# Performance work log

Hardware: AMD Instinct MI355X
Metric: run time of the kernel (lower is better)

Reference implementation:

```python
import jax, jax.numpy as jnp
import numpy as np

B, T, K = 256, 512, 128


def setup_inputs() -> dict:
    key = jax.random.key(0)
    k1, k2, k3, k4 = jax.random.split(key, 4)
    logits = jax.random.normal(k1, (B, T, K), dtype=jnp.float32)
    labels = jax.random.randint(k2, (B, T), 0, K, dtype=jnp.int32)
    seq_lens = jax.random.randint(k3, (B,), 1, T + 1, dtype=jnp.int32)
    trans = jax.random.uniform(k4, (K, K), dtype=jnp.float32)
    return {"logits": logits, "labels": labels, "seq_lens": seq_lens, "trans": trans}


def _crf_neg_log_likelihood(logits, labels, seq_lens, trans):
    # logits: [B,T,K], labels: [B,T] int, seq_lens: [B] int, trans: [K,K]
    Bb, Tt, Kk = logits.shape
    mask = (jnp.arange(Tt)[None, :] < seq_lens[:, None])  # [B,T] bool

    # ---- gold sequence score ----
    unary = jnp.take_along_axis(logits, labels[..., None].astype(jnp.int32), axis=-1)[..., 0]  # [B,T]
    unary_score = jnp.sum(jnp.where(mask, unary, 0.0), axis=-1)  # [B]
    pair = trans[labels[:, :-1], labels[:, 1:]]  # [B,T-1]
    pair_score = jnp.sum(jnp.where(mask[:, 1:], pair, 0.0), axis=-1)  # [B]
    score = unary_score + pair_score  # [B]

    # ---- log partition via forward algorithm (lax.scan over time) ----
    alpha0 = logits[:, 0]  # [B,K]
    xs = (jnp.swapaxes(logits[:, 1:], 0, 1), jnp.swapaxes(mask[:, 1:], 0, 1))  # [T-1,B,K],[T-1,B]

    def step(alpha, x):
        logit_t, m_t = x
        # alpha[:, :, None] + trans[None] : [B, K_prev, K_next]
        new = jax.nn.logsumexp(alpha[:, :, None] + trans[None, :, :], axis=1) + logit_t
        alpha = jnp.where(m_t[:, None], new, alpha)
        return alpha, None

    alpha, _ = jax.lax.scan(step, alpha0, xs)
    log_z = jax.nn.logsumexp(alpha, axis=-1)  # [B]

    log_likelihood = score - log_z
    return jnp.sum(-log_likelihood)  # scalar, matches tf.reduce_sum(-ll)


def reference(logits, labels, seq_lens, trans):
    return _crf_neg_log_likelihood(logits, labels, seq_lens, trans)
```

## Files before the change

kernel.cpp:

```cpp
#include <hip/hip_runtime.h>

#define Bdim 256
#define Tdim 512
#define Kdim 128
#define NT   128
#define CHUNK 8

typedef float v2f __attribute__((ext_vector_type(2)));

#define BAR() asm volatile("s_waitcnt lgkmcnt(0)\n\ts_barrier" ::: "memory")

template <int CTRL>
__device__ __forceinline__ float dpp_add(float v) {
    int r = __builtin_amdgcn_update_dpp(0, __float_as_int(v), CTRL, 0xF, 0xF, true);
    return v + __int_as_float(r);
}

__global__ __launch_bounds__(NT) __attribute__((amdgpu_waves_per_eu(1, 1)))
void crf_nll_kernel(
    const float* __restrict__ logits,
    const int*   __restrict__ labels,
    const int*   __restrict__ seq_lens,
    const float* __restrict__ trans,
    float* __restrict__ out)
{
    const int b   = blockIdx.x;
    const int tid = threadIdx.x;
    const int j   = tid >> 2;
    const int g   = tid & 3;
    const int L   = seq_lens[b];

    __shared__ float pbuf[2][Kdim];
    __shared__ float red2[NT / 64];

    const int*   lab_b   = labels + (size_t)b * Tdim;
    const float* logit_b = logits + (size_t)b * Tdim * Kdim;

    v2f e01[8][4], e23[8][4];
    #pragma unroll
    for (int ii = 0; ii < 8; ++ii) {
        const int f4 = (g << 3) + ((ii + j) & 7);
        #pragma unroll
        for (int ci = 0; ci < 4; ++ci) {
            const float4 tr =
                *(const float4*)&trans[(size_t)(4 * f4 + ci) * Kdim + 4 * j];
            e01[ii][ci] = (v2f){__expf(tr.x), __expf(tr.y)};
            e23[ii][ci] = (v2f){__expf(tr.z), __expf(tr.w)};
        }
    }

    float s = 0.f;
    #pragma unroll
    for (int t0 = 0; t0 < Tdim; t0 += NT) {
        const int t = t0 + tid;
        if (t < L) {
            const int lb = lab_b[t];
            s += logit_b[(size_t)t * Kdim + lb];
            if (t >= 1) s += trans[(size_t)lab_b[t - 1] * Kdim + lb];
        }
    }
    #pragma unroll
    for (int o = 32; o > 0; o >>= 1) s += __shfl_down(s, o, 64);
    if ((tid & 63) == 0) red2[tid >> 6] = s;

    pbuf[0][tid] = __expf(logit_b[tid]);
    float off = 0.f;
    int cb = 0;
    __syncthreads();
    const float score = red2[0] + red2[1];

    float curl[CHUNK], nxtl[CHUNK], ex[CHUNK];
    #pragma unroll
    for (int u = 0; u < CHUNK; ++u) {
        const int tt = 1 + u;
        curl[u] = (tt < Tdim) ? logit_b[(size_t)tt * Kdim + tid] : 0.f;
    }

#define STEP_BODY(SC_EXPR, RENORM)                                          \
    do {                                                                    \
        const float4* a4 = (const float4*)pbuf[cb];                         \
        float p0 = 1.f;                                                     \
        if (RENORM) p0 = pbuf[cb][0];                                       \
        v2f A0 = {0.f, 0.f}, A1 = {0.f, 0.f};                               \
        v2f B0 = {0.f, 0.f}, B1 = {0.f, 0.f};                               \
        _Pragma("unroll")                                                   \
        for (int ii = 0; ii < 8; ++ii) {                                    \
            const float4 p = a4[(g << 3) + ((ii + j) & 7)];                 \
            A0 = __builtin_elementwise_fma((v2f){p.x, p.x}, e01[ii][0], A0);\
            A1 = __builtin_elementwise_fma((v2f){p.x, p.x}, e23[ii][0], A1);\
            B0 = __builtin_elementwise_fma((v2f){p.y, p.y}, e01[ii][1], B0);\
            B1 = __builtin_elementwise_fma((v2f){p.y, p.y}, e23[ii][1], B1);\
            A0 = __builtin_elementwise_fma((v2f){p.z, p.z}, e01[ii][2], A0);\
            A1 = __builtin_elementwise_fma((v2f){p.z, p.z}, e23[ii][2], A1);\
            B0 = __builtin_elementwise_fma((v2f){p.w, p.w}, e01[ii][3], B0);\
            B1 = __builtin_elementwise_fma((v2f){p.w, p.w}, e23[ii][3], B1);\
        }                                                                   \
        const v2f s01 = A0 + B0;            \
        const v2f s23 = A1 + B1;            \
        float c0 = s01.x, c1 = s01.y, c2 = s23.x, c3 = s23.y;               \
        c0 = dpp_add<0xB1>(c0); c0 = dpp_add<0x4E>(c0);                     \
        c1 = dpp_add<0xB1>(c1); c1 = dpp_add<0x4E>(c1);                     \
        c2 = dpp_add<0xB1>(c2); c2 = dpp_add<0x4E>(c2);                     \
        c3 = dpp_add<0xB1>(c3); c3 = dpp_add<0x4E>(c3);                     \
        float sel  = (g & 1) ? c1 : c0;                                     \
        float selh = (g & 1) ? c3 : c2;                                     \
        sel = (g & 2) ? selh : sel;                                         \
        float anew = sel * (SC_EXPR);                                       \
        if (RENORM) {                                                       \
            const float lp0 = __logf(p0);                                   \
            anew *= __expf(-lp0);                                           \
            off  += lp0;                                                    \
        }                                                                   \
        pbuf[cb ^ 1][tid] = anew;                                           \
        cb ^= 1;                                                            \
        BAR();                                                              \
    } while (0)

    int tb = 1;
    for (; tb + CHUNK <= L; tb += CHUNK) {
        #pragma unroll
        for (int u = 0; u < CHUNK; ++u) {
            const int tt = tb + CHUNK + u;
            nxtl[u] = (tt < Tdim) ? logit_b[(size_t)tt * Kdim + tid] : 0.f;
        }
        #pragma unroll
        for (int u = 0; u < CHUNK; ++u)
            ex[u] = __expf(curl[u]);
        #pragma unroll
        for (int u = 0; u < CHUNK; ++u)
            STEP_BODY(ex[u], (u & 3) == 3);
        #pragma unroll
        for (int u = 0; u < CHUNK; ++u) curl[u] = nxtl[u];
    }
    for (int u = 0; tb + u < L; ++u)
        STEP_BODY(__expf(curl[u]), (u & 3) == 3);

#undef STEP_BODY

    __syncthreads();
    float as = pbuf[cb][tid];
    #pragma unroll
    for (int o = 32; o > 0; o >>= 1) as += __shfl_down(as, o, 64);
    __syncthreads();
    if ((tid & 63) == 0) red2[tid >> 6] = as;
    __syncthreads();
    if (tid == 0) {
        const float logz = off + __logf(red2[0] + red2[1]);
        atomicAdd(out, logz - score);
    }
}

extern "C" void kernel_launch(void* const* d_in, const int* in_sizes, int n_in,
                              void* d_out, int out_size, void* d_ws, size_t ws_size,
                              hipStream_t stream) {
    const float* logits   = (const float*)d_in[0];
    const int*   labels   = (const int*)d_in[1];
    const int*   seq_lens = (const int*)d_in[2];
    const float* trans    = (const float*)d_in[3];
    float* out = (float*)d_out;

    (void)hipMemsetAsync(out, 0, sizeof(float), stream);
    crf_nll_kernel<<<dim3(Bdim), dim3(NT), 0, stream>>>(
        logits, labels, seq_lens, trans, out);
}
```

Baseline: 268.1 us.

## Split each output column across eight lanes with 256 threads per block

Doubles the block to 256 threads so each column's 128-wide dot product is split across 8 lanes instead of 4. Each thread now holds half as many exp(trans) registers and does half the FMAs and LDS reads per step, which should shorten the serial per-timestep critical path. In exchange it adds a third DPP reduction stage, duplicate lanes that compute the same column, and a barrier spanning four waves instead of two.

```diff
diff --git a/kernel.cpp b/kernel.cpp
--- a/kernel.cpp
+++ b/kernel.cpp
@@ -3,7 +3,7 @@
 #define Bdim 256
 #define Tdim 512
 #define Kdim 128
-#define NT   128
+#define NT   256
 #define CHUNK 8
 
 typedef float v2f __attribute__((ext_vector_type(2)));
@@ -26,24 +26,25 @@
 {
     const int b   = blockIdx.x;
     const int tid = threadIdx.x;
-    const int j   = tid >> 2;
-    const int g   = tid & 3;
+    const int j4  = tid >> 3;
+    const int g   = tid & 7;
+    const int cj  = 4 * j4 + (g & 3);
     const int L   = seq_lens[b];
 
     __shared__ float pbuf[2][Kdim];
-    __shared__ float red2[NT / 64];
+    __shared__ float sred[NT / 64];
 
     const int*   lab_b   = labels + (size_t)b * Tdim;
     const float* logit_b = logits + (size_t)b * Tdim * Kdim;
 
-    v2f e01[8][4], e23[8][4];
+    v2f e01[4][4], e23[4][4];
     #pragma unroll
-    for (int ii = 0; ii < 8; ++ii) {
-        const int f4 = (g << 3) + ((ii + j) & 7);
+    for (int ii = 0; ii < 4; ++ii) {
+        const int row0 = 16 * g + (((ii + (g >> 1)) & 3) << 2);
         #pragma unroll
         for (int ci = 0; ci < 4; ++ci) {
             const float4 tr =
-                *(const float4*)&trans[(size_t)(4 * f4 + ci) * Kdim + 4 * j];
+                *(const float4*)&trans[(size_t)(row0 + ci) * Kdim + 4 * j4];
             e01[ii][ci] = (v2f){__expf(tr.x), __expf(tr.y)};
             e23[ii][ci] = (v2f){__expf(tr.z), __expf(tr.w)};
         }
@@ -61,19 +62,24 @@
     }
     #pragma unroll
     for (int o = 32; o > 0; o >>= 1) s += __shfl_down(s, o, 64);
-    if ((tid & 63) == 0) red2[tid >> 6] = s;
+    if ((tid & 63) == 0) sred[tid >> 6] = s;
 
-    pbuf[0][tid] = __expf(logit_b[tid]);
+    if (g < 4) pbuf[0][cj] = __expf(logit_b[cj]);
     float off = 0.f;
     int cb = 0;
     __syncthreads();
-    const float score = red2[0] + red2[1];
+
+    float score = 0.f;
+    if (tid == 0) {
+        #pragma unroll
+        for (int w = 0; w < NT / 64; ++w) score += sred[w];
+    }
 
     float curl[CHUNK], nxtl[CHUNK], ex[CHUNK];
     #pragma unroll
     for (int u = 0; u < CHUNK; ++u) {
         const int tt = 1 + u;
-        curl[u] = (tt < Tdim) ? logit_b[(size_t)tt * Kdim + tid] : 0.f;
+        curl[u] = (tt < Tdim) ? logit_b[(size_t)tt * Kdim + cj] : 0.f;
     }
 
 #define STEP_BODY(SC_EXPR, RENORM)                                          \
@@ -84,8 +90,8 @@
         v2f A0 = {0.f, 0.f}, A1 = {0.f, 0.f};                               \
         v2f B0 = {0.f, 0.f}, B1 = {0.f, 0.f};                               \
         _Pragma("unroll")                                                   \
-        for (int ii = 0; ii < 8; ++ii) {                                    \
-            const float4 p = a4[(g << 3) + ((ii + j) & 7)];                 \
+        for (int ii = 0; ii < 4; ++ii) {                                    \
+            const float4 p = a4[(g << 2) + ((ii + (g >> 1)) & 3)];          \
             A0 = __builtin_elementwise_fma((v2f){p.x, p.x}, e01[ii][0], A0);\
             A1 = __builtin_elementwise_fma((v2f){p.x, p.x}, e23[ii][0], A1);\
             B0 = __builtin_elementwise_fma((v2f){p.y, p.y}, e01[ii][1], B0);\
@@ -95,13 +101,13 @@
             B0 = __builtin_elementwise_fma((v2f){p.w, p.w}, e01[ii][3], B0);\
             B1 = __builtin_elementwise_fma((v2f){p.w, p.w}, e23[ii][3], B1);\
         }                                                                   \
-        const v2f s01 = A0 + B0;            \
-        const v2f s23 = A1 + B1;            \
+        const v2f s01 = A0 + B0;                   \
+        const v2f s23 = A1 + B1;                   \
         float c0 = s01.x, c1 = s01.y, c2 = s23.x, c3 = s23.y;               \
-        c0 = dpp_add<0xB1>(c0); c0 = dpp_add<0x4E>(c0);                     \
-        c1 = dpp_add<0xB1>(c1); c1 = dpp_add<0x4E>(c1);                     \
-        c2 = dpp_add<0xB1>(c2); c2 = dpp_add<0x4E>(c2);                     \
-        c3 = dpp_add<0xB1>(c3); c3 = dpp_add<0x4E>(c3);                     \
+        c0 = dpp_add<0xB1>(c0); c0 = dpp_add<0x4E>(c0); c0 = dpp_add<0x141>(c0);\
+        c1 = dpp_add<0xB1>(c1); c1 = dpp_add<0x4E>(c1); c1 = dpp_add<0x141>(c1);\
+        c2 = dpp_add<0xB1>(c2); c2 = dpp_add<0x4E>(c2); c2 = dpp_add<0x141>(c2);\
+        c3 = dpp_add<0xB1>(c3); c3 = dpp_add<0x4E>(c3); c3 = dpp_add<0x141>(c3);\
         float sel  = (g & 1) ? c1 : c0;                                     \
         float selh = (g & 1) ? c3 : c2;                                     \
         sel = (g & 2) ? selh : sel;                                         \
@@ -111,7 +117,7 @@
             anew *= __expf(-lp0);                                           \
             off  += lp0;                                                    \
         }                                                                   \
-        pbuf[cb ^ 1][tid] = anew;                                           \
+        if (g < 4) pbuf[cb ^ 1][cj] = anew;                                 \
         cb ^= 1;                                                            \
         BAR();                                                              \
     } while (0)
@@ -121,7 +127,7 @@
         #pragma unroll
         for (int u = 0; u < CHUNK; ++u) {
             const int tt = tb + CHUNK + u;
-            nxtl[u] = (tt < Tdim) ? logit_b[(size_t)tt * Kdim + tid] : 0.f;
+            nxtl[u] = (tt < Tdim) ? logit_b[(size_t)tt * Kdim + cj] : 0.f;
         }
         #pragma unroll
         for (int u = 0; u < CHUNK; ++u)
@@ -138,14 +144,17 @@
 #undef STEP_BODY
 
     __syncthreads();
-    float as = pbuf[cb][tid];
+    float as = (tid < Kdim) ? pbuf[cb][tid] : 0.f;
     #pragma unroll
     for (int o = 32; o > 0; o >>= 1) as += __shfl_down(as, o, 64);
     __syncthreads();
-    if ((tid & 63) == 0) red2[tid >> 6] = as;
+    if ((tid & 63) == 0) sred[tid >> 6] = as;
     __syncthreads();
     if (tid == 0) {
-        const float logz = off + __logf(red2[0] + red2[1]);
+        float tot = 0.f;
+        #pragma unroll
+        for (int w = 0; w < NT / 64; ++w) tot += sred[w];
+        const float logz = off + __logf(tot);
         atomicAdd(out, logz - score);
     }
 }
```

Result: faster. 237.2 us (-11.5%).
